# Kernel tuning notes

Measured on AMD Instinct MI355X. Metric: run time of the kernel, lower is better.

## Reference

```python
import jax, jax.numpy as jnp
import numpy as np

IN_CH = 256
OUT_CH = 256
RED = 4
QK = OUT_CH // RED  # 64


def setup_inputs() -> dict:
    key = jax.random.key(0)
    ks = jax.random.split(key, 7)
    s = 1.0 / np.sqrt(IN_CH)
    return {
        "x": jax.random.normal(ks[0], (8, IN_CH, 64, 64), dtype=jnp.float32),
        "w_q": jax.random.uniform(ks[1], (QK, IN_CH), jnp.float32, -s, s),
        "b_q": jax.random.uniform(ks[2], (QK,), jnp.float32, -s, s),
        "w_k": jax.random.uniform(ks[3], (QK, IN_CH), jnp.float32, -s, s),
        "b_k": jax.random.uniform(ks[4], (QK,), jnp.float32, -s, s),
        "w_v": jax.random.uniform(ks[5], (OUT_CH, IN_CH), jnp.float32, -s, s),
        "b_v": jax.random.uniform(ks[6], (OUT_CH,), jnp.float32, -s, s),
    }


def reference(x, w_q, b_q, w_k, b_k, w_v, b_v):
    B, C, H, W = x.shape
    xt = x.reshape(B, C, H * W)  # [B, C, N]
    # 1x1 convs == channel matmuls
    q = jnp.einsum('dc,bcn->bnd', w_q, xt) + b_q  # [B, N, QK]
    k = jnp.einsum('dc,bcn->bdn', w_k, xt) + b_k[:, None]  # [B, QK, N]
    v = jnp.einsum('dc,bcn->bnd', w_v, xt) + b_v  # [B, N, OUT]
    scores = jnp.einsum('bnd,bdm->bnm', q, k)  # [B, N, N], no scaling (as in source)
    attn = jax.nn.softmax(scores, axis=-1)
    out = jnp.einsum('bnm,bmd->bdn', attn, v)  # [B, OUT, N]
    return out.reshape(B, -1, H, W)
```

## Files before the change

kernel.cpp:

```cpp
#include <hip/hip_runtime.h>

typedef __bf16 bf16x8 __attribute__((ext_vector_type(8)));
typedef float f32x4 __attribute__((ext_vector_type(4)));
typedef unsigned int u32;
typedef u32 u32x4v __attribute__((ext_vector_type(4)));
typedef unsigned short u16;

#define LOG2E 1.44269504088896f

__device__ __forceinline__ u16 f2bf(float f){
  u32 b = __builtin_bit_cast(u32, f);
  b += 0x7FFFu + ((b >> 16) & 1u);
  return (u16)(b >> 16);
}

__global__ void prep_w(const float* __restrict__ wq, const float* __restrict__ wk,
                       const float* __restrict__ wv, u16* __restrict__ wfrag){
  int idx  = blockIdx.x * 256 + threadIdx.x;
  int e    = idx & 7;
  int lane = (idx >> 3) & 63;
  int f    = idx >> 9;
  int cc = f / 24, dt = f % 24;
  int d = dt * 16 + (lane & 15);
  int c = cc * 32 + (lane >> 4) * 8 + e;
  float v;
  if (d < 64)       v = wq[d * 256 + c];
  else if (d < 128) v = wk[(d - 64) * 256 + c];
  else              v = wv[(d - 128) * 256 + c];
  wfrag[idx] = f2bf(v);
}

__launch_bounds__(256, 2)
__global__ void proj_kernel(const float* __restrict__ x,
                            const float* __restrict__ bq, const float* __restrict__ bk,
                            const float* __restrict__ bv,
                            const u16* __restrict__ wfrag,
                            u16* __restrict__ qb, u16* __restrict__ kb, u16* __restrict__ vt)
{
  __shared__ u16 xlds[64 * 256];
  const int b    = blockIdx.x & 7;
  const int n0   = (blockIdx.x >> 3) * 64;
  const int t    = threadIdx.x;
  const int lane = t & 63;
  const int w    = t >> 6;
  const int g    = lane >> 4, j = lane & 15;

  {
    const int n = t & 63;
    const float* xp = x + ((size_t)b * 256) * 4096 + n0 + n;
    char* lbase = reinterpret_cast<char*>(xlds);
    #pragma unroll
    for (int pass = 0; pass < 8; ++pass){
      int c = pass * 32 + (t >> 6) * 8;
      float f0 = xp[(size_t)(c+0)*4096], f1 = xp[(size_t)(c+1)*4096];
      float f2 = xp[(size_t)(c+2)*4096], f3 = xp[(size_t)(c+3)*4096];
      float f4 = xp[(size_t)(c+4)*4096], f5 = xp[(size_t)(c+5)*4096];
      float f6 = xp[(size_t)(c+6)*4096], f7 = xp[(size_t)(c+7)*4096];
      uint4 q;
      q.x = (u32)f2bf(f0) | ((u32)f2bf(f1) << 16);
      q.y = (u32)f2bf(f2) | ((u32)f2bf(f3) << 16);
      q.z = (u32)f2bf(f4) | ((u32)f2bf(f5) << 16);
      q.w = (u32)f2bf(f6) | ((u32)f2bf(f7) << 16);
      u32 off = (u32)n * 512 + (((u32)c * 2) ^ (((u32)n & 31) << 4));
      *reinterpret_cast<uint4*>(lbase + off) = q;
    }
  }
  __syncthreads();

  f32x4 acc[6][4];
  #pragma unroll
  for (int i = 0; i < 6; ++i)
    #pragma unroll
    for (int nt = 0; nt < 4; ++nt) acc[i][nt] = f32x4{0.f,0.f,0.f,0.f};

  const char* lbase = reinterpret_cast<const char*>(xlds);
  for (int cc = 0; cc < 8; ++cc){
    bf16x8 a[6];
    #pragma unroll
    for (int i = 0; i < 6; ++i)
      a[i] = *reinterpret_cast<const bf16x8*>(wfrag + ((size_t)(cc*24 + w*6 + i) * 64 + lane) * 8);
    bf16x8 bb[4];
    #pragma unroll
    for (int nt = 0; nt < 4; ++nt){
      const u32 row = nt * 16 + j;
      const u32 off = row * 512 + (((u32)(cc * 64 + g * 16)) ^ ((row & 31) << 4));
      bb[nt] = *reinterpret_cast<const bf16x8*>(lbase + off);
    }
    #pragma unroll
    for (int i = 0; i < 6; ++i)
      #pragma unroll
      for (int nt = 0; nt < 4; ++nt)
        acc[i][nt] = __builtin_amdgcn_mfma_f32_16x16x32_bf16(a[i], bb[nt], acc[i][nt], 0, 0, 0);
  }

  #pragma unroll
  for (int i = 0; i < 6; ++i){
    const int dt = w * 6 + i;
    const int d0 = dt * 16;
    const int dd = d0 + 4 * g;
    if (d0 < 64){
      float b0 = bq[dd], b1 = bq[dd+1], b2 = bq[dd+2], b3 = bq[dd+3];
      #pragma unroll
      for (int nt = 0; nt < 4; ++nt){
        const int n = n0 + nt * 16 + j;
        uint2 u;
        u.x = (u32)f2bf((acc[i][nt][0] + b0) * LOG2E) | ((u32)f2bf((acc[i][nt][1] + b1) * LOG2E) << 16);
        u.y = (u32)f2bf((acc[i][nt][2] + b2) * LOG2E) | ((u32)f2bf((acc[i][nt][3] + b3) * LOG2E) << 16);
        *reinterpret_cast<uint2*>(qb + ((size_t)b * 4096 + n) * 64 + dd) = u;
      }
    } else if (d0 < 128){
      const int dk = dd - 64;
      float b0 = bk[dk], b1 = bk[dk+1], b2 = bk[dk+2], b3 = bk[dk+3];
      #pragma unroll
      for (int nt = 0; nt < 4; ++nt){
        const int n = n0 + nt * 16 + j;
        uint2 u;
        u.x = (u32)f2bf(acc[i][nt][0] + b0) | ((u32)f2bf(acc[i][nt][1] + b1) << 16);
        u.y = (u32)f2bf(acc[i][nt][2] + b2) | ((u32)f2bf(acc[i][nt][3] + b3) << 16);
        *reinterpret_cast<uint2*>(kb + ((size_t)b * 4096 + n) * 64 + dk) = u;
      }
    } else {
      const int dv = dd - 128;
      float b0 = bv[dv], b1 = bv[dv+1], b2 = bv[dv+2], b3 = bv[dv+3];
      #pragma unroll
      for (int nt = 0; nt < 4; ++nt){
        const int scol = ((nt & 2) << 4) | ((j & 12) << 1) | ((nt & 1) << 2) | (j & 3);
        const int n = n0 + scol;
        u16* vp = vt + (size_t)b * 256 * 4096 + n;
        vp[(size_t)(dv+0) * 4096] = f2bf(acc[i][nt][0] + b0);
        vp[(size_t)(dv+1) * 4096] = f2bf(acc[i][nt][1] + b1);
        vp[(size_t)(dv+2) * 4096] = f2bf(acc[i][nt][2] + b2);
        vp[(size_t)(dv+3) * 4096] = f2bf(acc[i][nt][3] + b3);
      }
    }
  }
}

__launch_bounds__(256, 2)
__global__ void attn_kernel(const u16* __restrict__ qb, const u16* __restrict__ kb,
                            const u16* __restrict__ vt, float* __restrict__ out)
{
  __shared__ u16 kl[2][64 * 64];
  __shared__ u16 vl[2][256 * 64];

  const int b    = blockIdx.x & 7;
  const int qc   = blockIdx.x >> 3;
  const int t    = threadIdx.x, lane = t & 63, w = t >> 6;
  const int g    = lane >> 4, j = lane & 15;

  const u16* Kg = kb + (size_t)b * 4096 * 64;
  const u16* Vg = vt + (size_t)b * 256 * 4096;

  const u16* Qrow = qb + ((size_t)b * 4096 + qc * 64 + w * 16 + j) * 64;
  const bf16x8 qf0 = *reinterpret_cast<const bf16x8*>(Qrow + 8 * g);
  const bf16x8 qf1 = *reinterpret_cast<const bf16x8*>(Qrow + 32 + 8 * g);

  f32x4 o[16];
  #pragma unroll
  for (int i = 0; i < 16; ++i) o[i] = f32x4{0.f,0.f,0.f,0.f};
  float mrun = -1.0e30f, lrun = 0.f;

  auto stage = [&](int tile, int buf){
    const int m0 = tile * 64;
    #pragma unroll
    for (int i = 0; i < 2; ++i){
      const int r = i * 32 + w * 8 + (lane >> 3);
      const char* src = reinterpret_cast<const char*>(Kg + (size_t)(m0 + r) * 64)
                        + ((((u32)lane & 7) * 16) ^ ((((u32)r) & 7) << 4));
      char* dst = reinterpret_cast<char*>(&kl[buf][0]) + i * 4096 + w * 1024;
      __builtin_amdgcn_global_load_lds((const __attribute__((address_space(1))) void*)src,
                                       (__attribute__((address_space(3))) void*)dst, 16, 0, 0);
    }
    #pragma unroll
    for (int i = 0; i < 8; ++i){
      const int dv = i * 32 + w * 8 + (lane >> 3);
      const char* src = reinterpret_cast<const char*>(Vg + (size_t)dv * 4096 + m0)
                        + ((((u32)lane & 7) * 16) ^ (((u32)dv & 7) << 4));
      char* dst = reinterpret_cast<char*>(&vl[buf][0]) + i * 4096 + w * 1024;
      __builtin_amdgcn_global_load_lds((const __attribute__((address_space(1))) void*)src,
                                       (__attribute__((address_space(3))) void*)dst, 16, 0, 0);
    }
  };

  stage(0, 0);
  __syncthreads();

  const u32 vsw = ((u32)j & 7) << 4;

  for (int tile = 0; tile < 64; ++tile){
    const int cur = tile & 1;
    if (tile + 1 < 64) stage(tile + 1, cur ^ 1);

    const char* kbase = reinterpret_cast<const char*>(&kl[cur][0]);
    const char* vbase = reinterpret_cast<const char*>(&vl[cur][0]);

    f32x4 s[4];
    __builtin_amdgcn_s_setprio(1);
    #pragma unroll
    for (int mt = 0; mt < 4; ++mt){
      const u32 row = mt * 16 + j;
      const u32 sw  = (row & 7) << 4;
      bf16x8 ka0 = *reinterpret_cast<const bf16x8*>(kbase + row * 128 + (((u32)(g * 16)) ^ sw));
      bf16x8 ka1 = *reinterpret_cast<const bf16x8*>(kbase + row * 128 + (((u32)(64 + g * 16)) ^ sw));
      f32x4 z = f32x4{0.f,0.f,0.f,0.f};
      z = __builtin_amdgcn_mfma_f32_16x16x32_bf16(ka0, qf0, z, 0, 0, 0);
      z = __builtin_amdgcn_mfma_f32_16x16x32_bf16(ka1, qf1, z, 0, 0, 0);
      s[mt] = z;
    }
    __builtin_amdgcn_s_setprio(0);

    float pmax = s[0][0];
    #pragma unroll
    for (int mt = 0; mt < 4; ++mt)
      #pragma unroll
      for (int r = 0; r < 4; ++r) pmax = fmaxf(pmax, s[mt][r]);
    pmax = fmaxf(pmax, __shfl_xor(pmax, 16));
    pmax = fmaxf(pmax, __shfl_xor(pmax, 32));

    if (__any(pmax > mrun + 8.0f)){
      const float mnew  = fmaxf(mrun, pmax);
      const float alpha = __builtin_amdgcn_exp2f(mrun - mnew);
      mrun = mnew;
      lrun *= alpha;
      #pragma unroll
      for (int i = 0; i < 16; ++i){
        o[i][0] *= alpha; o[i][1] *= alpha; o[i][2] *= alpha; o[i][3] *= alpha;
      }
    }

    float psum = 0.f;
    u32 pk[8];
    #pragma unroll
    for (int mt = 0; mt < 4; ++mt){
      float p0 = __builtin_amdgcn_exp2f(s[mt][0] - mrun);
      float p1 = __builtin_amdgcn_exp2f(s[mt][1] - mrun);
      float p2 = __builtin_amdgcn_exp2f(s[mt][2] - mrun);
      float p3 = __builtin_amdgcn_exp2f(s[mt][3] - mrun);
      psum += (p0 + p1) + (p2 + p3);
      pk[2*mt]   = (u32)f2bf(p0) | ((u32)f2bf(p1) << 16);
      pk[2*mt+1] = (u32)f2bf(p2) | ((u32)f2bf(p3) << 16);
    }
    psum += __shfl_xor(psum, 16);
    psum += __shfl_xor(psum, 32);
    lrun += psum;

    __builtin_amdgcn_s_setprio(1);
    #pragma unroll
    for (int mc = 0; mc < 2; ++mc){
      u32x4v pw = { pk[4*mc+0], pk[4*mc+1], pk[4*mc+2], pk[4*mc+3] };
      bf16x8 pf = __builtin_bit_cast(bf16x8, pw);
      #pragma unroll
      for (int dt = 0; dt < 16; ++dt){
        const u32 dv = dt * 16 + j;
        bf16x8 vf = *reinterpret_cast<const bf16x8*>(vbase + dv * 128 + (((u32)(mc * 64 + 16 * g)) ^ vsw));
        o[dt] = __builtin_amdgcn_mfma_f32_16x16x32_bf16(vf, pf, o[dt], 0, 0, 0);
      }
    }
    __builtin_amdgcn_s_setprio(0);

    __syncthreads();
  }

  const float rinv = 1.0f / lrun;
  const int n = qc * 64 + w * 16 + j;
  float* ob = out + (size_t)b * 256 * 4096 + n;
  #pragma unroll
  for (int dt = 0; dt < 16; ++dt){
    const int dv0 = dt * 16 + 4 * g;
    #pragma unroll
    for (int r = 0; r < 4; ++r)
      ob[(size_t)(dv0 + r) * 4096] = o[dt][r] * rinv;
  }
}

extern "C" void kernel_launch(void* const* d_in, const int* in_sizes, int n_in,
                              void* d_out, int out_size, void* d_ws, size_t ws_size,
                              hipStream_t stream)
{
  (void)in_sizes; (void)n_in; (void)out_size; (void)ws_size;
  const float* x  = (const float*)d_in[0];
  const float* wq = (const float*)d_in[1];
  const float* bq = (const float*)d_in[2];
  const float* wk = (const float*)d_in[3];
  const float* bk = (const float*)d_in[4];
  const float* wv = (const float*)d_in[5];
  const float* bv = (const float*)d_in[6];
  float* out = (float*)d_out;

  char* ws = (char*)d_ws;
  u16* qbuf  = (u16*)(ws + 0);
  u16* kbuf  = (u16*)(ws + 4194304);
  u16* vbuf  = (u16*)(ws + 8388608);
  u16* wfrag = (u16*)(ws + 25165824);

  prep_w<<<dim3(384), dim3(256), 0, stream>>>(wq, wk, wv, wfrag);
  proj_kernel<<<dim3(512), dim3(256), 0, stream>>>(x, bq, bk, bv, wfrag, qbuf, kbuf, vbuf);
  attn_kernel<<<dim3(512), dim3(256), 0, stream>>>(qbuf, kbuf, vbuf, out);
}
```

Measured before the change: 221.6 us.

## Split attention warps over query pairs and V halves; widen projection tiles

The attention kernel now gives each warp two 16-query groups and half of the 256 value channels, instead of one 16-query group and all channels. Each V fragment read from LDS therefore feeds two MFMAs, halving V LDS traffic per output, at the cost of computing QK^T scores twice across warp pairs. The projection kernel now processes 128 columns per block with half as many blocks, to reuse weight fragments more. Hand-written float-to-bf16 rounding is replaced with native bf16 conversions.

```diff
diff --git a/kernel.cpp b/kernel.cpp
--- a/kernel.cpp
+++ b/kernel.cpp
@@ -1,17 +1,16 @@
 #include <hip/hip_runtime.h>
 
 typedef __bf16 bf16x8 __attribute__((ext_vector_type(8)));
+typedef __bf16 bf16x2 __attribute__((ext_vector_type(2)));
 typedef float f32x4 __attribute__((ext_vector_type(4)));
 typedef unsigned int u32;
-typedef u32 u32x4v __attribute__((ext_vector_type(4)));
 typedef unsigned short u16;
 
 #define LOG2E 1.44269504088896f
 
-__device__ __forceinline__ u16 f2bf(float f){
-  u32 b = __builtin_bit_cast(u32, f);
-  b += 0x7FFFu + ((b >> 16) & 1u);
-  return (u16)(b >> 16);
+__device__ __forceinline__ u32 pk2(float a, float b){
+  bf16x2 v; v[0] = (__bf16)a; v[1] = (__bf16)b;
+  return __builtin_bit_cast(u32, v);
 }
 
 __global__ void prep_w(const float* __restrict__ wq, const float* __restrict__ wk,
@@ -27,51 +26,50 @@
   if (d < 64)       v = wq[d * 256 + c];
   else if (d < 128) v = wk[(d - 64) * 256 + c];
   else              v = wv[(d - 128) * 256 + c];
-  wfrag[idx] = f2bf(v);
-}
-
-__launch_bounds__(256, 2)
+  __bf16 h = (__bf16)v;
+  wfrag[idx] = __builtin_bit_cast(u16, h);
+}
+
+__launch_bounds__(256, 1)
 __global__ void proj_kernel(const float* __restrict__ x,
                             const float* __restrict__ bq, const float* __restrict__ bk,
                             const float* __restrict__ bv,
                             const u16* __restrict__ wfrag,
                             u16* __restrict__ qb, u16* __restrict__ kb, u16* __restrict__ vt)
 {
-  __shared__ u16 xlds[64 * 256];
+  __shared__ u16 xlds[128 * 256];
   const int b    = blockIdx.x & 7;
-  const int n0   = (blockIdx.x >> 3) * 64;
+  const int n0   = (blockIdx.x >> 3) * 128;
   const int t    = threadIdx.x;
   const int lane = t & 63;
   const int w    = t >> 6;
   const int g    = lane >> 4, j = lane & 15;
 
   {
-    const int n = t & 63;
+    const int n  = t & 127;
+    const int ch = t >> 7;
     const float* xp = x + ((size_t)b * 256) * 4096 + n0 + n;
     char* lbase = reinterpret_cast<char*>(xlds);
     #pragma unroll
-    for (int pass = 0; pass < 8; ++pass){
-      int c = pass * 32 + (t >> 6) * 8;
+    for (int pass = 0; pass < 16; ++pass){
+      int c = ch * 128 + pass * 8;
       float f0 = xp[(size_t)(c+0)*4096], f1 = xp[(size_t)(c+1)*4096];
       float f2 = xp[(size_t)(c+2)*4096], f3 = xp[(size_t)(c+3)*4096];
       float f4 = xp[(size_t)(c+4)*4096], f5 = xp[(size_t)(c+5)*4096];
       float f6 = xp[(size_t)(c+6)*4096], f7 = xp[(size_t)(c+7)*4096];
       uint4 q;
-      q.x = (u32)f2bf(f0) | ((u32)f2bf(f1) << 16);
-      q.y = (u32)f2bf(f2) | ((u32)f2bf(f3) << 16);
-      q.z = (u32)f2bf(f4) | ((u32)f2bf(f5) << 16);
-      q.w = (u32)f2bf(f6) | ((u32)f2bf(f7) << 16);
+      q.x = pk2(f0, f1); q.y = pk2(f2, f3); q.z = pk2(f4, f5); q.w = pk2(f6, f7);
       u32 off = (u32)n * 512 + (((u32)c * 2) ^ (((u32)n & 31) << 4));
       *reinterpret_cast<uint4*>(lbase + off) = q;
     }
   }
   __syncthreads();
 
-  f32x4 acc[6][4];
+  f32x4 acc[6][8];
   #pragma unroll
   for (int i = 0; i < 6; ++i)
     #pragma unroll
-    for (int nt = 0; nt < 4; ++nt) acc[i][nt] = f32x4{0.f,0.f,0.f,0.f};
+    for (int nt = 0; nt < 8; ++nt) acc[i][nt] = f32x4{0.f,0.f,0.f,0.f};
 
   const char* lbase = reinterpret_cast<const char*>(xlds);
   for (int cc = 0; cc < 8; ++cc){
@@ -79,9 +77,9 @@
     #pragma unroll
     for (int i = 0; i < 6; ++i)
       a[i] = *reinterpret_cast<const bf16x8*>(wfrag + ((size_t)(cc*24 + w*6 + i) * 64 + lane) * 8);
-    bf16x8 bb[4];
-    #pragma unroll
-    for (int nt = 0; nt < 4; ++nt){
+    bf16x8 bb[8];
+    #pragma unroll
+    for (int nt = 0; nt < 8; ++nt){
       const u32 row = nt * 16 + j;
       const u32 off = row * 512 + (((u32)(cc * 64 + g * 16)) ^ ((row & 31) << 4));
       bb[nt] = *reinterpret_cast<const bf16x8*>(lbase + off);
@@ -89,7 +87,7 @@
     #pragma unroll
     for (int i = 0; i < 6; ++i)
       #pragma unroll
-      for (int nt = 0; nt < 4; ++nt)
+      for (int nt = 0; nt < 8; ++nt)
         acc[i][nt] = __builtin_amdgcn_mfma_f32_16x16x32_bf16(a[i], bb[nt], acc[i][nt], 0, 0, 0);
   }
 
@@ -101,36 +99,41 @@
     if (d0 < 64){
       float b0 = bq[dd], b1 = bq[dd+1], b2 = bq[dd+2], b3 = bq[dd+3];
       #pragma unroll
-      for (int nt = 0; nt < 4; ++nt){
+      for (int nt = 0; nt < 8; ++nt){
         const int n = n0 + nt * 16 + j;
         uint2 u;
-        u.x = (u32)f2bf((acc[i][nt][0] + b0) * LOG2E) | ((u32)f2bf((acc[i][nt][1] + b1) * LOG2E) << 16);
-        u.y = (u32)f2bf((acc[i][nt][2] + b2) * LOG2E) | ((u32)f2bf((acc[i][nt][3] + b3) * LOG2E) << 16);
+        u.x = pk2((acc[i][nt][0] + b0) * LOG2E, (acc[i][nt][1] + b1) * LOG2E);
+        u.y = pk2((acc[i][nt][2] + b2) * LOG2E, (acc[i][nt][3] + b3) * LOG2E);
         *reinterpret_cast<uint2*>(qb + ((size_t)b * 4096 + n) * 64 + dd) = u;
       }
     } else if (d0 < 128){
       const int dk = dd - 64;
       float b0 = bk[dk], b1 = bk[dk+1], b2 = bk[dk+2], b3 = bk[dk+3];
       #pragma unroll
-      for (int nt = 0; nt < 4; ++nt){
+      for (int nt = 0; nt < 8; ++nt){
         const int n = n0 + nt * 16 + j;
         uint2 u;
-        u.x = (u32)f2bf(acc[i][nt][0] + b0) | ((u32)f2bf(acc[i][nt][1] + b1) << 16);
-        u.y = (u32)f2bf(acc[i][nt][2] + b2) | ((u32)f2bf(acc[i][nt][3] + b3) << 16);
+        u.x = pk2(acc[i][nt][0] + b0, acc[i][nt][1] + b1);
+        u.y = pk2(acc[i][nt][2] + b2, acc[i][nt][3] + b3);
         *reinterpret_cast<uint2*>(kb + ((size_t)b * 4096 + n) * 64 + dk) = u;
       }
     } else {
       const int dv = dd - 128;
       float b0 = bv[dv], b1 = bv[dv+1], b2 = bv[dv+2], b3 = bv[dv+3];
       #pragma unroll
-      for (int nt = 0; nt < 4; ++nt){
-        const int scol = ((nt & 2) << 4) | ((j & 12) << 1) | ((nt & 1) << 2) | (j & 3);
-        const int n = n0 + scol;
+      for (int nt = 0; nt < 8; ++nt){
+        const int nt4 = nt & 3;
+        const int scol = ((nt4 & 2) << 4) | ((j & 12) << 1) | ((nt4 & 1) << 2) | (j & 3);
+        const int n = n0 + (nt >> 2) * 64 + scol;
         u16* vp = vt + (size_t)b * 256 * 4096 + n;
-        vp[(size_t)(dv+0) * 4096] = f2bf(acc[i][nt][0] + b0);
-        vp[(size_t)(dv+1) * 4096] = f2bf(acc[i][nt][1] + b1);
-        vp[(size_t)(dv+2) * 4096] = f2bf(acc[i][nt][2] + b2);
-        vp[(size_t)(dv+3) * 4096] = f2bf(acc[i][nt][3] + b3);
+        __bf16 h0 = (__bf16)(acc[i][nt][0] + b0);
+        __bf16 h1 = (__bf16)(acc[i][nt][1] + b1);
+        __bf16 h2 = (__bf16)(acc[i][nt][2] + b2);
+        __bf16 h3 = (__bf16)(acc[i][nt][3] + b3);
+        vp[(size_t)(dv+0) * 4096] = __builtin_bit_cast(u16, h0);
+        vp[(size_t)(dv+1) * 4096] = __builtin_bit_cast(u16, h1);
+        vp[(size_t)(dv+2) * 4096] = __builtin_bit_cast(u16, h2);
+        vp[(size_t)(dv+3) * 4096] = __builtin_bit_cast(u16, h3);
       }
     }
   }
@@ -147,18 +150,25 @@
   const int qc   = blockIdx.x >> 3;
   const int t    = threadIdx.x, lane = t & 63, w = t >> 6;
   const int g    = lane >> 4, j = lane & 15;
+  const int colh = w & 1;
+  const int dvh  = (w >> 1) * 128;
 
   const u16* Kg = kb + (size_t)b * 4096 * 64;
   const u16* Vg = vt + (size_t)b * 256 * 4096;
 
-  const u16* Qrow = qb + ((size_t)b * 4096 + qc * 64 + w * 16 + j) * 64;
-  const bf16x8 qf0 = *reinterpret_cast<const bf16x8*>(Qrow + 8 * g);
-  const bf16x8 qf1 = *reinterpret_cast<const bf16x8*>(Qrow + 32 + 8 * g);
-
-  f32x4 o[16];
-  #pragma unroll
-  for (int i = 0; i < 16; ++i) o[i] = f32x4{0.f,0.f,0.f,0.f};
-  float mrun = -1.0e30f, lrun = 0.f;
+  bf16x8 qf[2][2];
+  #pragma unroll
+  for (int ng = 0; ng < 2; ++ng){
+    const u16* Qrow = qb + ((size_t)b * 4096 + qc * 64 + colh * 32 + ng * 16 + j) * 64;
+    qf[ng][0] = *reinterpret_cast<const bf16x8*>(Qrow + 8 * g);
+    qf[ng][1] = *reinterpret_cast<const bf16x8*>(Qrow + 32 + 8 * g);
+  }
+
+  f32x4 o[8][2];
+  #pragma unroll
+  for (int i = 0; i < 8; ++i){ o[i][0] = f32x4{0.f,0.f,0.f,0.f}; o[i][1] = f32x4{0.f,0.f,0.f,0.f}; }
+  float mrun[2] = {-1.0e30f, -1.0e30f};
+  float lrun[2] = {0.f, 0.f};
 
   auto stage = [&](int tile, int buf){
     const int m0 = tile * 64;
@@ -194,7 +204,7 @@
     const char* kbase = reinterpret_cast<const char*>(&kl[cur][0]);
     const char* vbase = reinterpret_cast<const char*>(&vl[cur][0]);
 
-    f32x4 s[4];
+    f32x4 s[2][4];
     __builtin_amdgcn_s_setprio(1);
     #pragma unroll
     for (int mt = 0; mt < 4; ++mt){
@@ -202,58 +212,74 @@
       const u32 sw  = (row & 7) << 4;
       bf16x8 ka0 = *reinterpret_cast<const bf16x8*>(kbase + row * 128 + (((u32)(g * 16)) ^ sw));
       bf16x8 ka1 = *reinterpret_cast<const bf16x8*>(kbase + row * 128 + (((u32)(64 + g * 16)) ^ sw));
-      f32x4 z = f32x4{0.f,0.f,0.f,0.f};
-      z = __builtin_amdgcn_mfma_f32_16x16x32_bf16(ka0, qf0, z, 0, 0, 0);
-      z = __builtin_amdgcn_mfma_f32_16x16x32_bf16(ka1, qf1, z, 0, 0, 0);
-      s[mt] = z;
+      #pragma unroll
+      for (int ng = 0; ng < 2; ++ng){
+        f32x4 z = f32x4{0.f,0.f,0.f,0.f};
+        z = __builtin_amdgcn_mfma_f32_16x16x32_bf16(ka0, qf[ng][0], z, 0, 0, 0);
+        z = __builtin_amdgcn_mfma_f32_16x16x32_bf16(ka1, qf[ng][1], z, 0, 0, 0);
+        s[ng][mt] = z;
+      }
     }
     __builtin_amdgcn_s_setprio(0);
 
-    float pmax = s[0][0];
-    #pragma unroll
-    for (int mt = 0; mt < 4; ++mt)
-      #pragma unroll
-      for (int r = 0; r < 4; ++r) pmax = fmaxf(pmax, s[mt][r]);
-    pmax = fmaxf(pmax, __shfl_xor(pmax, 16));
-    pmax = fmaxf(pmax, __shfl_xor(pmax, 32));
-
-    if (__any(pmax > mrun + 8.0f)){
-      const float mnew  = fmaxf(mrun, pmax);
-      const float alpha = __builtin_amdgcn_exp2f(mrun - mnew);
-      mrun = mnew;
-      lrun *= alpha;
-      #pragma unroll
-      for (int i = 0; i < 16; ++i){
-        o[i][0] *= alpha; o[i][1] *= alpha; o[i][2] *= alpha; o[i][3] *= alpha;
-      }
-    }
-
-    float psum = 0.f;
-    u32 pk[8];
-    #pragma unroll
-    for (int mt = 0; mt < 4; ++mt){
-      float p0 = __builtin_amdgcn_exp2f(s[mt][0] - mrun);
-      float p1 = __builtin_amdgcn_exp2f(s[mt][1] - mrun);
-      float p2 = __builtin_amdgcn_exp2f(s[mt][2] - mrun);
-      float p3 = __builtin_amdgcn_exp2f(s[mt][3] - mrun);
-      psum += (p0 + p1) + (p2 + p3);
-      pk[2*mt]   = (u32)f2bf(p0) | ((u32)f2bf(p1) << 16);
-      pk[2*mt+1] = (u32)f2bf(p2) | ((u32)f2bf(p3) << 16);
-    }
-    psum += __shfl_xor(psum, 16);
-    psum += __shfl_xor(psum, 32);
-    lrun += psum;
+    float pmax[2];
+    #pragma unroll
+    for (int ng = 0; ng < 2; ++ng){
+      float pm = s[ng][0][0];
+      #pragma unroll
+      for (int mt = 0; mt < 4; ++mt)
+        #pragma unroll
+        for (int r = 0; r < 4; ++r) pm = fmaxf(pm, s[ng][mt][r]);
+      pm = fmaxf(pm, __shfl_xor(pm, 16));
+      pm = fmaxf(pm, __shfl_xor(pm, 32));
+      pmax[ng] = pm;
+    }
+
+    if (__any((pmax[0] > mrun[0] + 8.0f) || (pmax[1] > mrun[1] + 8.0f))){
+      #pragma unroll
+      for (int ng = 0; ng < 2; ++ng){
+        const float mnew  = fmaxf(mrun[ng], pmax[ng]);
+        const float alpha = __builtin_amdgcn_exp2f(mrun[ng] - mnew);
+        mrun[ng] = mnew;
+        lrun[ng] *= alpha;
+        #pragma unroll
+        for (int i = 0; i < 8; ++i){
+          o[i][ng][0] *= alpha; o[i][ng][1] *= alpha;
+          o[i][ng][2] *= alpha; o[i][ng][3] *= alpha;
+        }
+      }
+    }
+
+    bf16x8 pf[2][2];
+    #pragma unroll
+    for (int ng = 0; ng < 2; ++ng){
+      float psum = 0.f;
+      #pragma unroll
+      for (int mt = 0; mt < 4; ++mt){
+        float p0 = __builtin_amdgcn_exp2f(s[ng][mt][0] - mrun[ng]);
+        float p1 = __builtin_amdgcn_exp2f(s[ng][mt][1] - mrun[ng]);
+        float p2 = __builtin_amdgcn_exp2f(s[ng][mt][2] - mrun[ng]);
+        float p3 = __builtin_amdgcn_exp2f(s[ng][mt][3] - mrun[ng]);
+        psum += (p0 + p1) + (p2 + p3);
+        pf[ng][mt >> 1][(mt & 1) * 4 + 0] = (__bf16)p0;
+        pf[ng][mt >> 1][(mt & 1) * 4 + 1] = (__bf16)p1;
+        pf[ng][mt >> 1][(mt & 1) * 4 + 2] = (__bf16)p2;
+        pf[ng][mt >> 1][(mt & 1) * 4 + 3] = (__bf16)p3;
+      }
+      psum += __shfl_xor(psum, 16);
+      psum += __shfl_xor(psum, 32);
+      lrun[ng] += psum;
+    }
 
     __builtin_amdgcn_s_setprio(1);
     #pragma unroll
     for (int mc = 0; mc < 2; ++mc){
-      u32x4v pw = { pk[4*mc+0], pk[4*mc+1], pk[4*mc+2], pk[4*mc+3] };
-      bf16x8 pf = __builtin_bit_cast(bf16x8, pw);
-      #pragma unroll
-      for (int dt = 0; dt < 16; ++dt){
-        const u32 dv = dt * 16 + j;
+      #pragma unroll
+      for (int dt = 0; dt < 8; ++dt){
+        const u32 dv = dvh + dt * 16 + j;
         bf16x8 vf = *reinterpret_cast<const bf16x8*>(vbase + dv * 128 + (((u32)(mc * 64 + 16 * g)) ^ vsw));
-        o[dt] = __builtin_amdgcn_mfma_f32_16x16x32_bf16(vf, pf, o[dt], 0, 0, 0);
+        o[dt][0] = __builtin_amdgcn_mfma_f32_16x16x32_bf16(vf, pf[0][mc], o[dt][0], 0, 0, 0);
+        o[dt][1] = __builtin_amdgcn_mfma_f32_16x16x32_bf16(vf, pf[1][mc], o[dt][1], 0, 0, 0);
       }
     }
     __builtin_amdgcn_s_setprio(0);
@@ -261,15 +287,18 @@
     __syncthreads();
   }
 
-  const float rinv = 1.0f / lrun;
-  const int n = qc * 64 + w * 16 + j;
-  float* ob = out + (size_t)b * 256 * 4096 + n;
-  #pragma unroll
-  for (int dt = 0; dt < 16; ++dt){
-    const int dv0 = dt * 16 + 4 * g;
-    #pragma unroll
-    for (int r = 0; r < 4; ++r)
-      ob[(size_t)(dv0 + r) * 4096] = o[dt][r] * rinv;
+  #pragma unroll
+  for (int ng = 0; ng < 2; ++ng){
+    const float rinv = 1.0f / lrun[ng];
+    const int n = qc * 64 + colh * 32 + ng * 16 + j;
+    float* ob = out + (size_t)b * 256 * 4096 + n;
+    #pragma unroll
+    for (int dt = 0; dt < 8; ++dt){
+      const int dv0 = dvh + dt * 16 + 4 * g;
+      #pragma unroll
+      for (int r = 0; r < 4; ++r)
+        ob[(size_t)(dv0 + r) * 4096] = o[dt][ng][r] * rinv;
+    }
   }
 }
 
@@ -294,6 +323,6 @@
   u16* wfrag = (u16*)(ws + 25165824);
 
   prep_w<<<dim3(384), dim3(256), 0, stream>>>(wq, wk, wv, wfrag);
-  proj_kernel<<<dim3(512), dim3(256), 0, stream>>>(x, bq, bk, bv, wfrag, qbuf, kbuf, vbuf);
+  proj_kernel<<<dim3(256), dim3(256), 0, stream>>>(x, bq, bk, bv, wfrag, qbuf, kbuf, vbuf);
   attn_kernel<<<dim3(512), dim3(256), 0, stream>>>(qbuf, kbuf, vbuf, out);
 }
```

Result: no change. 225.6 us (+1.8%).

## Split attention across 8 waves by value-channel halves and use native bf16 conversion

Applied to the files above, without the earlier changes.

Both projection and attention kernels move to 512-thread blocks. In attention, waves pair up on the same query rows and each computes half of the 256 output channels, halving accumulator registers per wave at the cost of duplicating the QK score and softmax computation. Projection gives each wave half as many output tiles. Manual bf16 rounding is replaced with compiler bf16 casts that can map to packed hardware conversion instructions.

```diff
diff --git a/kernel.cpp b/kernel.cpp
--- a/kernel.cpp
+++ b/kernel.cpp
@@ -1,6 +1,7 @@
 #include <hip/hip_runtime.h>
 
 typedef __bf16 bf16x8 __attribute__((ext_vector_type(8)));
+typedef __bf16 bf16x2 __attribute__((ext_vector_type(2)));
 typedef float f32x4 __attribute__((ext_vector_type(4)));
 typedef unsigned int u32;
 typedef u32 u32x4v __attribute__((ext_vector_type(4)));
@@ -8,10 +9,9 @@
 
 #define LOG2E 1.44269504088896f
 
-__device__ __forceinline__ u16 f2bf(float f){
-  u32 b = __builtin_bit_cast(u32, f);
-  b += 0x7FFFu + ((b >> 16) & 1u);
-  return (u16)(b >> 16);
+__device__ __forceinline__ u32 pk2(float a, float b){
+  bf16x2 v; v[0] = (__bf16)a; v[1] = (__bf16)b;
+  return __builtin_bit_cast(u32, v);
 }
 
 __global__ void prep_w(const float* __restrict__ wq, const float* __restrict__ wk,
@@ -27,10 +27,11 @@
   if (d < 64)       v = wq[d * 256 + c];
   else if (d < 128) v = wk[(d - 64) * 256 + c];
   else              v = wv[(d - 128) * 256 + c];
-  wfrag[idx] = f2bf(v);
-}
-
-__launch_bounds__(256, 2)
+  __bf16 h = (__bf16)v;
+  wfrag[idx] = __builtin_bit_cast(u16, h);
+}
+
+__launch_bounds__(512, 4)
 __global__ void proj_kernel(const float* __restrict__ x,
                             const float* __restrict__ bq, const float* __restrict__ bk,
                             const float* __restrict__ bv,
@@ -46,39 +47,37 @@
   const int g    = lane >> 4, j = lane & 15;
 
   {
-    const int n = t & 63;
+    const int n  = t & 63;
+    const int ch = t >> 6;
     const float* xp = x + ((size_t)b * 256) * 4096 + n0 + n;
     char* lbase = reinterpret_cast<char*>(xlds);
     #pragma unroll
-    for (int pass = 0; pass < 8; ++pass){
-      int c = pass * 32 + (t >> 6) * 8;
+    for (int pass = 0; pass < 4; ++pass){
+      int c = pass * 64 + ch * 8;
       float f0 = xp[(size_t)(c+0)*4096], f1 = xp[(size_t)(c+1)*4096];
       float f2 = xp[(size_t)(c+2)*4096], f3 = xp[(size_t)(c+3)*4096];
       float f4 = xp[(size_t)(c+4)*4096], f5 = xp[(size_t)(c+5)*4096];
       float f6 = xp[(size_t)(c+6)*4096], f7 = xp[(size_t)(c+7)*4096];
       uint4 q;
-      q.x = (u32)f2bf(f0) | ((u32)f2bf(f1) << 16);
-      q.y = (u32)f2bf(f2) | ((u32)f2bf(f3) << 16);
-      q.z = (u32)f2bf(f4) | ((u32)f2bf(f5) << 16);
-      q.w = (u32)f2bf(f6) | ((u32)f2bf(f7) << 16);
+      q.x = pk2(f0, f1); q.y = pk2(f2, f3); q.z = pk2(f4, f5); q.w = pk2(f6, f7);
       u32 off = (u32)n * 512 + (((u32)c * 2) ^ (((u32)n & 31) << 4));
       *reinterpret_cast<uint4*>(lbase + off) = q;
     }
   }
   __syncthreads();
 
-  f32x4 acc[6][4];
+  f32x4 acc[3][4];
   #pragma unroll
-  for (int i = 0; i < 6; ++i)
+  for (int i = 0; i < 3; ++i)
     #pragma unroll
     for (int nt = 0; nt < 4; ++nt) acc[i][nt] = f32x4{0.f,0.f,0.f,0.f};
 
   const char* lbase = reinterpret_cast<const char*>(xlds);
   for (int cc = 0; cc < 8; ++cc){
-    bf16x8 a[6];
-    #pragma unroll
-    for (int i = 0; i < 6; ++i)
-      a[i] = *reinterpret_cast<const bf16x8*>(wfrag + ((size_t)(cc*24 + w*6 + i) * 64 + lane) * 8);
+    bf16x8 a[3];
+    #pragma unroll
+    for (int i = 0; i < 3; ++i)
+      a[i] = *reinterpret_cast<const bf16x8*>(wfrag + ((size_t)(cc*24 + w*3 + i) * 64 + lane) * 8);
     bf16x8 bb[4];
     #pragma unroll
     for (int nt = 0; nt < 4; ++nt){
@@ -87,15 +86,15 @@
       bb[nt] = *reinterpret_cast<const bf16x8*>(lbase + off);
     }
     #pragma unroll
-    for (int i = 0; i < 6; ++i)
+    for (int i = 0; i < 3; ++i)
       #pragma unroll
       for (int nt = 0; nt < 4; ++nt)
         acc[i][nt] = __builtin_amdgcn_mfma_f32_16x16x32_bf16(a[i], bb[nt], acc[i][nt], 0, 0, 0);
   }
 
   #pragma unroll
-  for (int i = 0; i < 6; ++i){
-    const int dt = w * 6 + i;
+  for (int i = 0; i < 3; ++i){
+    const int dt = w * 3 + i;
     const int d0 = dt * 16;
     const int dd = d0 + 4 * g;
     if (d0 < 64){
@@ -104,8 +103,8 @@
       for (int nt = 0; nt < 4; ++nt){
         const int n = n0 + nt * 16 + j;
         uint2 u;
-        u.x = (u32)f2bf((acc[i][nt][0] + b0) * LOG2E) | ((u32)f2bf((acc[i][nt][1] + b1) * LOG2E) << 16);
-        u.y = (u32)f2bf((acc[i][nt][2] + b2) * LOG2E) | ((u32)f2bf((acc[i][nt][3] + b3) * LOG2E) << 16);
+        u.x = pk2((acc[i][nt][0] + b0) * LOG2E, (acc[i][nt][1] + b1) * LOG2E);
+        u.y = pk2((acc[i][nt][2] + b2) * LOG2E, (acc[i][nt][3] + b3) * LOG2E);
         *reinterpret_cast<uint2*>(qb + ((size_t)b * 4096 + n) * 64 + dd) = u;
       }
     } else if (d0 < 128){
@@ -115,8 +114,8 @@
       for (int nt = 0; nt < 4; ++nt){
         const int n = n0 + nt * 16 + j;
         uint2 u;
-        u.x = (u32)f2bf(acc[i][nt][0] + b0) | ((u32)f2bf(acc[i][nt][1] + b1) << 16);
-        u.y = (u32)f2bf(acc[i][nt][2] + b2) | ((u32)f2bf(acc[i][nt][3] + b3) << 16);
+        u.x = pk2(acc[i][nt][0] + b0, acc[i][nt][1] + b1);
+        u.y = pk2(acc[i][nt][2] + b2, acc[i][nt][3] + b3);
         *reinterpret_cast<uint2*>(kb + ((size_t)b * 4096 + n) * 64 + dk) = u;
       }
     } else {
@@ -127,16 +126,20 @@
         const int scol = ((nt & 2) << 4) | ((j & 12) << 1) | ((nt & 1) << 2) | (j & 3);
         const int n = n0 + scol;
         u16* vp = vt + (size_t)b * 256 * 4096 + n;
-        vp[(size_t)(dv+0) * 4096] = f2bf(acc[i][nt][0] + b0);
-        vp[(size_t)(dv+1) * 4096] = f2bf(acc[i][nt][1] + b1);
-        vp[(size_t)(dv+2) * 4096] = f2bf(acc[i][nt][2] + b2);
-        vp[(size_t)(dv+3) * 4096] = f2bf(acc[i][nt][3] + b3);
-      }
-    }
-  }
-}
-
-__launch_bounds__(256, 2)
+        __bf16 h0 = (__bf16)(acc[i][nt][0] + b0);
+        __bf16 h1 = (__bf16)(acc[i][nt][1] + b1);
+        __bf16 h2 = (__bf16)(acc[i][nt][2] + b2);
+        __bf16 h3 = (__bf16)(acc[i][nt][3] + b3);
+        vp[(size_t)(dv+0) * 4096] = __builtin_bit_cast(u16, h0);
+        vp[(size_t)(dv+1) * 4096] = __builtin_bit_cast(u16, h1);
+        vp[(size_t)(dv+2) * 4096] = __builtin_bit_cast(u16, h2);
+        vp[(size_t)(dv+3) * 4096] = __builtin_bit_cast(u16, h3);
+      }
+    }
+  }
+}
+
+__launch_bounds__(512, 4)
 __global__ void attn_kernel(const u16* __restrict__ qb, const u16* __restrict__ kb,
                             const u16* __restrict__ vt, float* __restrict__ out)
 {
@@ -147,36 +150,37 @@
   const int qc   = blockIdx.x >> 3;
   const int t    = threadIdx.x, lane = t & 63, w = t >> 6;
   const int g    = lane >> 4, j = lane & 15;
+  const int colq = w & 3;
+  const int dvh  = (w >> 2) * 128;
 
   const u16* Kg = kb + (size_t)b * 4096 * 64;
   const u16* Vg = vt + (size_t)b * 256 * 4096;
 
-  const u16* Qrow = qb + ((size_t)b * 4096 + qc * 64 + w * 16 + j) * 64;
+  const u16* Qrow = qb + ((size_t)b * 4096 + qc * 64 + colq * 16 + j) * 64;
   const bf16x8 qf0 = *reinterpret_cast<const bf16x8*>(Qrow + 8 * g);
   const bf16x8 qf1 = *reinterpret_cast<const bf16x8*>(Qrow + 32 + 8 * g);
 
-  f32x4 o[16];
+  f32x4 o[8];
   #pragma unroll
-  for (int i = 0; i < 16; ++i) o[i] = f32x4{0.f,0.f,0.f,0.f};
+  for (int i = 0; i < 8; ++i) o[i] = f32x4{0.f,0.f,0.f,0.f};
   float mrun = -1.0e30f, lrun = 0.f;
 
   auto stage = [&](int tile, int buf){
     const int m0 = tile * 64;
-    #pragma unroll
-    for (int i = 0; i < 2; ++i){
-      const int r = i * 32 + w * 8 + (lane >> 3);
+    {
+      const int r = w * 8 + (lane >> 3);
       const char* src = reinterpret_cast<const char*>(Kg + (size_t)(m0 + r) * 64)
                         + ((((u32)lane & 7) * 16) ^ ((((u32)r) & 7) << 4));
-      char* dst = reinterpret_cast<char*>(&kl[buf][0]) + i * 4096 + w * 1024;
+      char* dst = reinterpret_cast<char*>(&kl[buf][0]) + w * 1024;
       __builtin_amdgcn_global_load_lds((const __attribute__((address_space(1))) void*)src,
                                        (__attribute__((address_space(3))) void*)dst, 16, 0, 0);
     }
     #pragma unroll
-    for (int i = 0; i < 8; ++i){
-      const int dv = i * 32 + w * 8 + (lane >> 3);
+    for (int i = 0; i < 4; ++i){
+      const int dv = i * 64 + w * 8 + (lane >> 3);
       const char* src = reinterpret_cast<const char*>(Vg + (size_t)dv * 4096 + m0)
                         + ((((u32)lane & 7) * 16) ^ (((u32)dv & 7) << 4));
-      char* dst = reinterpret_cast<char*>(&vl[buf][0]) + i * 4096 + w * 1024;
+      char* dst = reinterpret_cast<char*>(&vl[buf][0]) + i * 8192 + w * 1024;
       __builtin_amdgcn_global_load_lds((const __attribute__((address_space(1))) void*)src,
                                        (__attribute__((address_space(3))) void*)dst, 16, 0, 0);
     }
@@ -223,13 +227,13 @@
       mrun = mnew;
       lrun *= alpha;
       #pragma unroll
-      for (int i = 0; i < 16; ++i){
+      for (int i = 0; i < 8; ++i){
         o[i][0] *= alpha; o[i][1] *= alpha; o[i][2] *= alpha; o[i][3] *= alpha;
       }
     }
 
     float psum = 0.f;
-    u32 pk[8];
+    u32 pw[8];
     #pragma unroll
     for (int mt = 0; mt < 4; ++mt){
       float p0 = __builtin_amdgcn_exp2f(s[mt][0] - mrun);
@@ -237,8 +241,8 @@
       float p2 = __builtin_amdgcn_exp2f(s[mt][2] - mrun);
       float p3 = __builtin_amdgcn_exp2f(s[mt][3] - mrun);
       psum += (p0 + p1) + (p2 + p3);
-      pk[2*mt]   = (u32)f2bf(p0) | ((u32)f2bf(p1) << 16);
-      pk[2*mt+1] = (u32)f2bf(p2) | ((u32)f2bf(p3) << 16);
+      pw[2*mt]   = pk2(p0, p1);
+      pw[2*mt+1] = pk2(p2, p3);
     }
     psum += __shfl_xor(psum, 16);
     psum += __shfl_xor(psum, 32);
@@ -247,11 +251,11 @@
     __builtin_amdgcn_s_setprio(1);
     #pragma unroll
     for (int mc = 0; mc < 2; ++mc){
-      u32x4v pw = { pk[4*mc+0], pk[4*mc+1], pk[4*mc+2], pk[4*mc+3] };
-      bf16x8 pf = __builtin_bit_cast(bf16x8, pw);
-      #pragma unroll
-      for (int dt = 0; dt < 16; ++dt){
-        const u32 dv = dt * 16 + j;
+      u32x4v pv = { pw[4*mc+0], pw[4*mc+1], pw[4*mc+2], pw[4*mc+3] };
+      bf16x8 pf = __builtin_bit_cast(bf16x8, pv);
+      #pragma unroll
+      for (int dt = 0; dt < 8; ++dt){
+        const u32 dv = dvh + dt * 16 + j;
         bf16x8 vf = *reinterpret_cast<const bf16x8*>(vbase + dv * 128 + (((u32)(mc * 64 + 16 * g)) ^ vsw));
         o[dt] = __builtin_amdgcn_mfma_f32_16x16x32_bf16(vf, pf, o[dt], 0, 0, 0);
       }
@@ -262,11 +266,11 @@
   }
 
   const float rinv = 1.0f / lrun;
-  const int n = qc * 64 + w * 16 + j;
+  const int n = qc * 64 + colq * 16 + j;
   float* ob = out + (size_t)b * 256 * 4096 + n;
   #pragma unroll
-  for (int dt = 0; dt < 16; ++dt){
-    const int dv0 = dt * 16 + 4 * g;
+  for (int dt = 0; dt < 8; ++dt){
+    const int dv0 = dvh + dt * 16 + 4 * g;
     #pragma unroll
     for (int r = 0; r < 4; ++r)
       ob[(size_t)(dv0 + r) * 4096] = o[dt][r] * rinv;
@@ -294,6 +298,6 @@
   u16* wfrag = (u16*)(ws + 25165824);
 
   prep_w<<<dim3(384), dim3(256), 0, stream>>>(wq, wk, wv, wfrag);
-  proj_kernel<<<dim3(512), dim3(256), 0, stream>>>(x, bq, bk, bv, wfrag, qbuf, kbuf, vbuf);
-  attn_kernel<<<dim3(512), dim3(256), 0, stream>>>(qbuf, kbuf, vbuf, out);
-}
+  proj_kernel<<<dim3(512), dim3(512), 0, stream>>>(x, bq, bk, bv, wfrag, qbuf, kbuf, vbuf);
+  attn_kernel<<<dim3(512), dim3(512), 0, stream>>>(qbuf, kbuf, vbuf, out);
+}
```

Result: slower. 228.8 us (+3.3%).
